# Optimization experiments

Hardware: AMD Instinct MI355X
Metric: run time of the kernel (lower is better)

Reference implementation:

```python
import jax, jax.numpy as jnp
import numpy as np

D = 1024  # model_embedding_dim
T = 512   # n_future_dx
B = 16384


def setup_inputs() -> dict:
    key = jax.random.key(0)
    k1, k2, k3, k4, k5 = jax.random.split(key, 5)
    x = jax.random.normal(k1, (B, D), dtype=jnp.float32)
    # Linear layers: torch nn.Linear stores weight [out, in], bias [out]
    s = 1.0 / np.sqrt(D)
    Wh = jax.random.uniform(k2, (T, D), jnp.float32, -s, s)
    bh = jax.random.uniform(k3, (T,), jnp.float32, -s, s)
    Wb = jax.random.uniform(k4, (1, D), jnp.float32, -s, s)
    bb = jax.random.uniform(k5, (1,), jnp.float32, -s, s)
    return {"x": x, "Wh": Wh, "bh": bh, "Wb": Wb, "bb": bb}


def reference(x, Wh, bh, Wb, bb):
    # hazards = relu(x @ Wh^T + bh)  -> [B, T]
    hazards = jax.nn.relu(jnp.einsum('bd,td->bt', x, Wh) + bh)
    # masked expand-and-sum with upper-triangular mask (mask[i,j]=1 iff i<=j)
    # equals inclusive prefix sum along T.
    cum = jnp.cumsum(hazards, axis=1)
    base = jnp.einsum('bd,od->bo', x, Wb) + bb  # [B, 1]
    return cum + base
```

## Files before the change

### kernel.cpp

```cpp
#include <hip/hip_runtime.h>
#include <hip/hip_bf16.h>


typedef __bf16 bf16x8 __attribute__((ext_vector_type(8)));
typedef __bf16 bf16x4 __attribute__((ext_vector_type(4)));
typedef float f32x4 __attribute__((ext_vector_type(4)));

#define BM 64
#define KC 256
#define NCH 4
#define TDIM 512
#define DDIM 1024
#define AROWB 512
#define ACHSZ (BM * AROWB)

__global__ __launch_bounds__(256) void cvt_wh_kernel(const float* __restrict__ src,
                                                     __bf16* __restrict__ dst) {
    const int i = (blockIdx.x * 256 + threadIdx.x) * 4;
    const float4 v = *reinterpret_cast<const float4*>(src + i);
    bf16x4 o;
    o[0] = (__bf16)v.x; o[1] = (__bf16)v.y; o[2] = (__bf16)v.z; o[3] = (__bf16)v.w;
    *reinterpret_cast<bf16x4*>(dst + i) = o;
}

__device__ __forceinline__ int aswz(int row, int slotByte) {
    return (slotByte ^ ((row & 7) << 4));
}

__global__ __launch_bounds__(512, 2) void survival_kernel(
    const float* __restrict__ x,
    const __bf16* __restrict__ Whb,
    const float* __restrict__ bh,
    const float* __restrict__ Wb,
    const float* __restrict__ bbp,
    float* __restrict__ out)
{
    __shared__ __align__(16) char Alds[2][ACHSZ];
    __shared__ float baseLds[BM];
    __shared__ float totLds[BM][8];

    const int tid  = threadIdx.x;
    const int lane = tid & 63;
    const int wid  = tid >> 6;
    const int brow = blockIdx.x * BM;
    const float bb0 = bbp[0];

    const int ar = tid >> 3;
    const int ac = tid & 7;
    const float* xrow = x + (size_t)(brow + ar) * DDIM + ac * 32;
    const float* wbp  = Wb + ac * 32;

    const int tcol = lane & 15;
    const int kq   = lane >> 4;
    const __bf16* bbase[4];
#pragma unroll
    for (int n = 0; n < 4; ++n)
        bbase[n] = Whb + (size_t)(wid * 64 + n * 16 + tcol) * DDIM + kq * 8;

    float bpart = 0.f;
    f32x4 acc[4][4];
#pragma unroll
    for (int rt = 0; rt < 4; ++rt)
#pragma unroll
        for (int n = 0; n < 4; ++n)
            acc[rt][n] = (f32x4){0.f, 0.f, 0.f, 0.f};

    float4 xs[8];

    auto issueX = [&](int c) {
#pragma unroll
        for (int j = 0; j < 8; ++j)
            xs[j] = *reinterpret_cast<const float4*>(xrow + c * KC + j * 4);
    };

    auto writeA = [&](int c, int buf) {
#pragma unroll
        for (int j = 0; j < 8; ++j) {
            const float4 wv = *reinterpret_cast<const float4*>(wbp + c * KC + j * 4);
            bpart += xs[j].x * wv.x + xs[j].y * wv.y + xs[j].z * wv.z + xs[j].w * wv.w;
        }
#pragma unroll
        for (int j2 = 0; j2 < 4; ++j2) {
            bf16x8 av;
            av[0] = (__bf16)xs[2*j2].x;   av[1] = (__bf16)xs[2*j2].y;
            av[2] = (__bf16)xs[2*j2].z;   av[3] = (__bf16)xs[2*j2].w;
            av[4] = (__bf16)xs[2*j2+1].x; av[5] = (__bf16)xs[2*j2+1].y;
            av[6] = (__bf16)xs[2*j2+1].z; av[7] = (__bf16)xs[2*j2+1].w;
            *reinterpret_cast<bf16x8*>(
                &Alds[buf][0] + ar * AROWB + aswz(ar, (ac * 4 + j2) * 16)) = av;
        }
    };

    auto computeC = [&](int c, int buf) {
        const char* Ab = &Alds[buf][0];
#pragma unroll
        for (int kst = 0; kst < 8; ++kst) {
            bf16x8 af[4];
#pragma unroll
            for (int rt = 0; rt < 4; ++rt) {
                const int row = rt * 16 + tcol;
                af[rt] = *reinterpret_cast<const bf16x8*>(
                    Ab + row * AROWB + aswz(row, kst * 64 + kq * 16));
            }
#pragma unroll
            for (int n = 0; n < 4; ++n) {
                const bf16x8 bfr = *reinterpret_cast<const bf16x8*>(
                    bbase[n] + c * KC + kst * 32);
#pragma unroll
                for (int rt = 0; rt < 4; ++rt)
                    acc[rt][n] = __builtin_amdgcn_mfma_f32_16x16x32_bf16(
                        af[rt], bfr, acc[rt][n], 0, 0, 0);
            }
        }
    };

    issueX(0);
    writeA(0, 0);
    __syncthreads();
#pragma unroll
    for (int c = 0; c < NCH; ++c) {
        if (c + 1 < NCH) issueX(c + 1);
        computeC(c, c & 1);
        if (c + 1 < NCH) writeA(c + 1, (c + 1) & 1);
        __syncthreads();
    }

    bpart += __shfl_xor(bpart, 1, 8);
    bpart += __shfl_xor(bpart, 2, 8);
    bpart += __shfl_xor(bpart, 4, 8);
    if (ac == 0) baseLds[ar] = bpart + bb0;

    float bhv[4];
#pragma unroll
    for (int n = 0; n < 4; ++n)
        bhv[n] = bh[wid * 64 + n * 16 + tcol];

    float carry[4][4];
#pragma unroll
    for (int rt = 0; rt < 4; ++rt)
#pragma unroll
        for (int j = 0; j < 4; ++j) carry[rt][j] = 0.f;

#pragma unroll
    for (int n = 0; n < 4; ++n) {
#pragma unroll
        for (int rt = 0; rt < 4; ++rt) {
#pragma unroll
            for (int j = 0; j < 4; ++j) {
                float v = fmaxf(acc[rt][n][j] + bhv[n], 0.f);
#pragma unroll
                for (int off = 1; off < 16; off <<= 1) {
                    const float u = __shfl_up(v, (unsigned)off, 16);
                    if ((lane & 15) >= off) v += u;
                }
                v += carry[rt][j];
                carry[rt][j] = __shfl(v, 15, 16);
                acc[rt][n][j] = v;
            }
        }
    }

    if (tcol == 0) {
#pragma unroll
        for (int rt = 0; rt < 4; ++rt)
#pragma unroll
            for (int j = 0; j < 4; ++j) {
                const int r = rt * 16 + kq * 4 + j;
                totLds[r][wid] = carry[rt][j];
            }
    }
    __syncthreads();

#pragma unroll
    for (int rt = 0; rt < 4; ++rt) {
#pragma unroll
        for (int j = 0; j < 4; ++j) {
            const int r = rt * 16 + kq * 4 + j;
            float rc = baseLds[r];
#pragma unroll
            for (int w = 0; w < 7; ++w)
                if (w < wid) rc += totLds[r][w];
            float* orow = out + (size_t)(brow + r) * TDIM + wid * 64 + tcol;
#pragma unroll
            for (int n = 0; n < 4; ++n)
                orow[n * 16] = acc[rt][n][j] + rc;
        }
    }
}

extern "C" void kernel_launch(void* const* d_in, const int* in_sizes, int n_in,
                              void* d_out, int out_size, void* d_ws, size_t ws_size,
                              hipStream_t stream) {
    const float* x  = (const float*)d_in[0];
    const float* Wh = (const float*)d_in[1];
    const float* bh = (const float*)d_in[2];
    const float* Wb = (const float*)d_in[3];
    const float* bb = (const float*)d_in[4];
    float* out = (float*)d_out;
    __bf16* Whb = (__bf16*)d_ws;

    cvt_wh_kernel<<<512, 256, 0, stream>>>(Wh, Whb);
    survival_kernel<<<256, 512, 0, stream>>>(x, Whb, bh, Wb, bb, out);
}
```

Measured before the change: 156.7 us.

## Pre-tile Wh into MFMA fragment layout and use 16-wave blocks

```diff
diff --git a/kernel.cpp b/kernel.cpp
--- a/kernel.cpp
+++ b/kernel.cpp
@@ -3,31 +3,33 @@
 
 
 typedef __bf16 bf16x8 __attribute__((ext_vector_type(8)));
-typedef __bf16 bf16x4 __attribute__((ext_vector_type(4)));
 typedef float f32x4 __attribute__((ext_vector_type(4)));
 
-#define BM 64
-#define KC 256
-#define NCH 4
 #define TDIM 512
 #define DDIM 1024
-#define AROWB 512
-#define ACHSZ (BM * AROWB)
-
-__global__ __launch_bounds__(256) void cvt_wh_kernel(const float* __restrict__ src,
-                                                     __bf16* __restrict__ dst) {
-    const int i = (blockIdx.x * 256 + threadIdx.x) * 4;
-    const float4 v = *reinterpret_cast<const float4*>(src + i);
-    bf16x4 o;
-    o[0] = (__bf16)v.x; o[1] = (__bf16)v.y; o[2] = (__bf16)v.z; o[3] = (__bf16)v.w;
-    *reinterpret_cast<bf16x4*>(dst + i) = o;
+#define BM 64
+#define NCH 4
+#define KS_PER_CH 8
+#define BLKE 512
+
+__global__ __launch_bounds__(256) void prep_wh(const float* __restrict__ src,
+                                               __bf16* __restrict__ dst) {
+    const int i    = blockIdx.x * 256 + threadIdx.x;
+    const int lane = i & 63;
+    const int blk  = i >> 6;
+    const int tt   = blk >> 5;
+    const int ks   = blk & 31;
+    const int row  = tt * 16 + (lane & 15);
+    const int k    = ks * 32 + (lane >> 4) * 8;
+    const float4 a = *reinterpret_cast<const float4*>(src + (size_t)row * DDIM + k);
+    const float4 b = *reinterpret_cast<const float4*>(src + (size_t)row * DDIM + k + 4);
+    bf16x8 o;
+    o[0] = (__bf16)a.x; o[1] = (__bf16)a.y; o[2] = (__bf16)a.z; o[3] = (__bf16)a.w;
+    o[4] = (__bf16)b.x; o[5] = (__bf16)b.y; o[6] = (__bf16)b.z; o[7] = (__bf16)b.w;
+    *reinterpret_cast<bf16x8*>(dst + (size_t)i * 8) = o;
 }
 
-__device__ __forceinline__ int aswz(int row, int slotByte) {
-    return (slotByte ^ ((row & 7) << 4));
-}
-
-__global__ __launch_bounds__(512, 2) void survival_kernel(
+__global__ __launch_bounds__(1024, 4) void survival_kernel(
     const float* __restrict__ x,
     const __bf16* __restrict__ Whb,
     const float* __restrict__ bh,
@@ -35,105 +37,106 @@
     const float* __restrict__ bbp,
     float* __restrict__ out)
 {
-    __shared__ __align__(16) char Alds[2][ACHSZ];
+    __shared__ __align__(16) char Abf[BM * 2048];
     __shared__ float baseLds[BM];
-    __shared__ float totLds[BM][8];
+    __shared__ float totLds[BM][16];
 
     const int tid  = threadIdx.x;
     const int lane = tid & 63;
     const int wid  = tid >> 6;
+    const int am   = lane & 15;
+    const int kq   = lane >> 4;
     const int brow = blockIdx.x * BM;
     const float bb0 = bbp[0];
 
-    const int ar = tid >> 3;
-    const int ac = tid & 7;
-    const float* xrow = x + (size_t)(brow + ar) * DDIM + ac * 32;
-    const float* wbp  = Wb + ac * 32;
-
-    const int tcol = lane & 15;
-    const int kq   = lane >> 4;
-    const __bf16* bbase[4];
-#pragma unroll
-    for (int n = 0; n < 4; ++n)
-        bbase[n] = Whb + (size_t)(wid * 64 + n * 16 + tcol) * DDIM + kq * 8;
+    const int ar = tid >> 4;
+    const int ap = tid & 15;
+    const float* xrow = x + (size_t)(brow + ar) * DDIM;
 
     float bpart = 0.f;
-    f32x4 acc[4][4];
+    f32x4 acc[4][2];
 #pragma unroll
     for (int rt = 0; rt < 4; ++rt)
 #pragma unroll
-        for (int n = 0; n < 4; ++n)
+        for (int n = 0; n < 2; ++n)
             acc[rt][n] = (f32x4){0.f, 0.f, 0.f, 0.f};
 
-    float4 xs[8];
-
-    auto issueX = [&](int c) {
-#pragma unroll
-        for (int j = 0; j < 8; ++j)
-            xs[j] = *reinterpret_cast<const float4*>(xrow + c * KC + j * 4);
+    float4 xs0, xs1, xs2, xs3;
+
+    auto issueFill = [&](int c) {
+        const int k0 = c * 256 + ap * 8;
+        xs0 = *reinterpret_cast<const float4*>(xrow + k0);
+        xs1 = *reinterpret_cast<const float4*>(xrow + k0 + 4);
+        xs2 = *reinterpret_cast<const float4*>(xrow + k0 + 128);
+        xs3 = *reinterpret_cast<const float4*>(xrow + k0 + 132);
     };
 
-    auto writeA = [&](int c, int buf) {
-#pragma unroll
-        for (int j = 0; j < 8; ++j) {
-            const float4 wv = *reinterpret_cast<const float4*>(wbp + c * KC + j * 4);
-            bpart += xs[j].x * wv.x + xs[j].y * wv.y + xs[j].z * wv.z + xs[j].w * wv.w;
-        }
-#pragma unroll
-        for (int j2 = 0; j2 < 4; ++j2) {
-            bf16x8 av;
-            av[0] = (__bf16)xs[2*j2].x;   av[1] = (__bf16)xs[2*j2].y;
-            av[2] = (__bf16)xs[2*j2].z;   av[3] = (__bf16)xs[2*j2].w;
-            av[4] = (__bf16)xs[2*j2+1].x; av[5] = (__bf16)xs[2*j2+1].y;
-            av[6] = (__bf16)xs[2*j2+1].z; av[7] = (__bf16)xs[2*j2+1].w;
-            *reinterpret_cast<bf16x8*>(
-                &Alds[buf][0] + ar * AROWB + aswz(ar, (ac * 4 + j2) * 16)) = av;
+    auto writeFill = [&](int c) {
+        const int k0 = c * 256 + ap * 8;
+        const float4 w0 = *reinterpret_cast<const float4*>(Wb + k0);
+        const float4 w1 = *reinterpret_cast<const float4*>(Wb + k0 + 4);
+        const float4 w2 = *reinterpret_cast<const float4*>(Wb + k0 + 128);
+        const float4 w3 = *reinterpret_cast<const float4*>(Wb + k0 + 132);
+        bpart += xs0.x*w0.x + xs0.y*w0.y + xs0.z*w0.z + xs0.w*w0.w
+               + xs1.x*w1.x + xs1.y*w1.y + xs1.z*w1.z + xs1.w*w1.w
+               + xs2.x*w2.x + xs2.y*w2.y + xs2.z*w2.z + xs2.w*w2.w
+               + xs3.x*w3.x + xs3.y*w3.y + xs3.z*w3.z + xs3.w*w3.w;
+        bf16x8 v0, v1;
+        v0[0]=(__bf16)xs0.x; v0[1]=(__bf16)xs0.y; v0[2]=(__bf16)xs0.z; v0[3]=(__bf16)xs0.w;
+        v0[4]=(__bf16)xs1.x; v0[5]=(__bf16)xs1.y; v0[6]=(__bf16)xs1.z; v0[7]=(__bf16)xs1.w;
+        v1[0]=(__bf16)xs2.x; v1[1]=(__bf16)xs2.y; v1[2]=(__bf16)xs2.z; v1[3]=(__bf16)xs2.w;
+        v1[4]=(__bf16)xs3.x; v1[5]=(__bf16)xs3.y; v1[6]=(__bf16)xs3.z; v1[7]=(__bf16)xs3.w;
+        const int s0 = c * 32 + ap;
+        const int s1 = s0 + 16;
+        *reinterpret_cast<bf16x8*>(&Abf[0] + ar * 2048 + ((s0 ^ (ar & 7)) * 16)) = v0;
+        *reinterpret_cast<bf16x8*>(&Abf[0] + ar * 2048 + ((s1 ^ (ar & 7)) * 16)) = v1;
+    };
+
+    const __bf16* bbase = Whb + (size_t)(wid * 2) * 32 * BLKE + (size_t)lane * 8;
+
+    auto computeChunk = [&](int c) {
+#pragma unroll
+        for (int s = 0; s < KS_PER_CH; ++s) {
+            const int ks = c * KS_PER_CH + s;
+            const bf16x8 b0 = *reinterpret_cast<const bf16x8*>(bbase + (size_t)ks * BLKE);
+            const bf16x8 b1 = *reinterpret_cast<const bf16x8*>(bbase + (size_t)(32 + ks) * BLKE);
+            bf16x8 af[4];
+#pragma unroll
+            for (int rt = 0; rt < 4; ++rt) {
+                const int row = rt * 16 + am;
+                const int slot = (ks * 4 + kq) ^ (am & 7);
+                af[rt] = *reinterpret_cast<const bf16x8*>(&Abf[0] + row * 2048 + slot * 16);
+            }
+            __builtin_amdgcn_s_setprio(1);
+#pragma unroll
+            for (int rt = 0; rt < 4; ++rt) {
+                acc[rt][0] = __builtin_amdgcn_mfma_f32_16x16x32_bf16(af[rt], b0, acc[rt][0], 0, 0, 0);
+                acc[rt][1] = __builtin_amdgcn_mfma_f32_16x16x32_bf16(af[rt], b1, acc[rt][1], 0, 0, 0);
+            }
+            __builtin_amdgcn_s_setprio(0);
         }
     };
 
-    auto computeC = [&](int c, int buf) {
-        const char* Ab = &Alds[buf][0];
-#pragma unroll
-        for (int kst = 0; kst < 8; ++kst) {
-            bf16x8 af[4];
-#pragma unroll
-            for (int rt = 0; rt < 4; ++rt) {
-                const int row = rt * 16 + tcol;
-                af[rt] = *reinterpret_cast<const bf16x8*>(
-                    Ab + row * AROWB + aswz(row, kst * 64 + kq * 16));
-            }
-#pragma unroll
-            for (int n = 0; n < 4; ++n) {
-                const bf16x8 bfr = *reinterpret_cast<const bf16x8*>(
-                    bbase[n] + c * KC + kst * 32);
-#pragma unroll
-                for (int rt = 0; rt < 4; ++rt)
-                    acc[rt][n] = __builtin_amdgcn_mfma_f32_16x16x32_bf16(
-                        af[rt], bfr, acc[rt][n], 0, 0, 0);
-            }
-        }
-    };
-
-    issueX(0);
-    writeA(0, 0);
+    issueFill(0);
+    writeFill(0);
     __syncthreads();
 #pragma unroll
     for (int c = 0; c < NCH; ++c) {
-        if (c + 1 < NCH) issueX(c + 1);
-        computeC(c, c & 1);
-        if (c + 1 < NCH) writeA(c + 1, (c + 1) & 1);
-        __syncthreads();
-    }
-
-    bpart += __shfl_xor(bpart, 1, 8);
-    bpart += __shfl_xor(bpart, 2, 8);
-    bpart += __shfl_xor(bpart, 4, 8);
-    if (ac == 0) baseLds[ar] = bpart + bb0;
-
-    float bhv[4];
-#pragma unroll
-    for (int n = 0; n < 4; ++n)
-        bhv[n] = bh[wid * 64 + n * 16 + tcol];
+        if (c + 1 < NCH) issueFill(c + 1);
+        computeChunk(c);
+        if (c + 1 < NCH) { writeFill(c + 1); __syncthreads(); }
+    }
+
+    bpart += __shfl_xor(bpart, 1, 16);
+    bpart += __shfl_xor(bpart, 2, 16);
+    bpart += __shfl_xor(bpart, 4, 16);
+    bpart += __shfl_xor(bpart, 8, 16);
+    if (ap == 0) baseLds[ar] = bpart + bb0;
+
+    float bhv[2];
+#pragma unroll
+    for (int n = 0; n < 2; ++n)
+        bhv[n] = bh[wid * 32 + n * 16 + am];
 
     float carry[4][4];
 #pragma unroll
@@ -142,7 +145,7 @@
         for (int j = 0; j < 4; ++j) carry[rt][j] = 0.f;
 
 #pragma unroll
-    for (int n = 0; n < 4; ++n) {
+    for (int n = 0; n < 2; ++n) {
 #pragma unroll
         for (int rt = 0; rt < 4; ++rt) {
 #pragma unroll
@@ -151,7 +154,7 @@
 #pragma unroll
                 for (int off = 1; off < 16; off <<= 1) {
                     const float u = __shfl_up(v, (unsigned)off, 16);
-                    if ((lane & 15) >= off) v += u;
+                    if (am >= off) v += u;
                 }
                 v += carry[rt][j];
                 carry[rt][j] = __shfl(v, 15, 16);
@@ -160,14 +163,12 @@
         }
     }
 
-    if (tcol == 0) {
+    if (am == 0) {
 #pragma unroll
         for (int rt = 0; rt < 4; ++rt)
 #pragma unroll
-            for (int j = 0; j < 4; ++j) {
-                const int r = rt * 16 + kq * 4 + j;
-                totLds[r][wid] = carry[rt][j];
-            }
+            for (int j = 0; j < 4; ++j)
+                totLds[rt * 16 + kq * 4 + j][wid] = carry[rt][j];
     }
     __syncthreads();
 
@@ -178,12 +179,11 @@
             const int r = rt * 16 + kq * 4 + j;
             float rc = baseLds[r];
 #pragma unroll
-            for (int w = 0; w < 7; ++w)
+            for (int w = 0; w < 15; ++w)
                 if (w < wid) rc += totLds[r][w];
-            float* orow = out + (size_t)(brow + r) * TDIM + wid * 64 + tcol;
-#pragma unroll
-            for (int n = 0; n < 4; ++n)
-                orow[n * 16] = acc[rt][n][j] + rc;
+            float* orow = out + (size_t)(brow + r) * TDIM + wid * 32 + am;
+            orow[0]  = acc[rt][0][j] + rc;
+            orow[16] = acc[rt][1][j] + rc;
         }
     }
 }
@@ -199,6 +199,6 @@
     float* out = (float*)d_out;
     __bf16* Whb = (__bf16*)d_ws;
 
-    cvt_wh_kernel<<<512, 256, 0, stream>>>(Wh, Whb);
-    survival_kernel<<<256, 512, 0, stream>>>(x, Whb, bh, Wb, bb, out);
+    prep_wh<<<256, 256, 0, stream>>>(Wh, Whb);
+    survival_kernel<<<256, 1024, 0, stream>>>(x, Whb, bh, Wb, bb, out);
 }
```

Result: faster. 133.8 us (-14.6%).
